# Kernel tuning notes

Hardware: AMD Instinct MI355X
Metric: run time of the kernel (lower is better)

The kernel has to match this reference:

```python
import jax, jax.numpy as jnp
import numpy as np


def setup_inputs() -> dict:
    key = jax.random.key(0)
    ks = jax.random.split(key, 6)
    B, L, D, E = 4, 2048, 1024, 4
    H = 4 * D
    x = jax.random.normal(ks[0], (B, L, D), dtype=jnp.float32)
    # router: Linear(D, 2D) -> GELU -> Linear(2D, E); kaiming-ish init
    rW1 = jax.random.normal(ks[1], (D, 2 * D), dtype=jnp.float32) * (2.0 / D) ** 0.5
    rb1 = jnp.zeros((2 * D,), dtype=jnp.float32)
    rW2 = jax.random.normal(ks[2], (2 * D, E), dtype=jnp.float32) * (2.0 / (2 * D)) ** 0.5
    rb2 = jnp.zeros((E,), dtype=jnp.float32)
    # experts: Linear(D, 4D) -> GELU -> Linear(4D, D), stacked over E
    We1 = jax.random.normal(ks[3], (E, D, H), dtype=jnp.float32) * (2.0 / D) ** 0.5
    be1 = jnp.zeros((E, H), dtype=jnp.float32)
    We2 = jax.random.normal(ks[4], (E, H, D), dtype=jnp.float32) * (2.0 / H) ** 0.5
    be2 = jnp.zeros((E, D), dtype=jnp.float32)
    return {"x": x, "rW1": rW1, "rb1": rb1, "rW2": rW2, "rb2": rb2,
            "We1": We1, "be1": be1, "We2": We2, "be2": be2}


def reference(x, rW1, rb1, rW2, rb2, We1, be1, We2, be2):
    E = We1.shape[0]
    top_k = min(2, E)
    # router (dropouts are identity in eval mode)
    rh = jax.nn.gelu(x @ rW1 + rb1, approximate=False)          # [B,L,2D]
    router_logits = rh @ rW2 + rb2                               # [B,L,E]
    router_probs = jax.nn.softmax(router_logits, axis=-1)
    expert_weights, expert_indices = jax.lax.top_k(router_probs, top_k)  # [B,L,k]
    one_hot = jax.nn.one_hot(expert_indices, E, dtype=x.dtype)   # [B,L,k,E]
    token_mask = one_hot.sum(axis=2)                             # [B,L,E] 1 if expert selected
    combine_w = (one_hot * expert_weights[..., None]).sum(axis=2)  # [B,L,E] gate weight per expert
    out = jnp.zeros_like(x)
    for e in range(E):  # fixed small expert count; dense per-expert MLP over all tokens (as original)
        xi = x * token_mask[..., e:e + 1]
        h = jax.nn.gelu(xi @ We1[e] + be1[e], approximate=False)  # [B,L,4D]
        yo = h @ We2[e] + be2[e]                                  # [B,L,D]
        out = out + yo * combine_w[..., e:e + 1]
    return out
```

## Files before the change

kernel.cpp:

```cpp
#include <hip/hip_runtime.h>
#include <math.h>


typedef short bf16x8 __attribute__((ext_vector_type(8)));
typedef float f32x4 __attribute__((ext_vector_type(4)));
typedef unsigned short u16;

__device__ __forceinline__ u16 f2bf(float f) {
  unsigned u = __float_as_uint(f);
  u += 0x7FFFu + ((u >> 16) & 1u);
  return (u16)(u >> 16);
}
__device__ __forceinline__ float bf2f(u16 s) {
  return __uint_as_float(((unsigned)s) << 16);
}
__device__ __forceinline__ float gelu_f(float x) {
  return 0.5f * x * (1.0f + erff(x * 0.70710678118654752f));
}
__device__ __forceinline__ float gelu_fast(float x) {
  float y = 1.5957691216057308f * (x + 0.044715f * x * x * x);
  float e = __expf(y);
  float t = 1.0f - 2.0f * __builtin_amdgcn_rcpf(e + 1.0f);
  return 0.5f * x * (1.0f + t);
}
__device__ __forceinline__ void gload_lds16(const void* g, void* l) {
  __builtin_amdgcn_global_load_lds(
      (const __attribute__((address_space(1))) void*)g,
      (__attribute__((address_space(3))) void*)l, 16, 0, 0);
}

__global__ __launch_bounds__(256) void convert_split_kernel(
    const float* __restrict__ in, u16* __restrict__ hi, u16* __restrict__ lo,
    int n4) {
  int i = blockIdx.x * blockDim.x + threadIdx.x;
  int stride = gridDim.x * blockDim.x;
  for (; i < n4; i += stride) {
    float4 v = ((const float4*)in)[i];
    float f[4] = {v.x, v.y, v.z, v.w};
    ushort4 h4, l4;
    u16* hp = (u16*)&h4;
    u16* lp = (u16*)&l4;
#pragma unroll
    for (int u = 0; u < 4; ++u) {
      u16 h = f2bf(f[u]);
      hp[u] = h;
      lp[u] = f2bf(f[u] - bf2f(h));
    }
    ((ushort4*)hi)[i] = h4;
    ((ushort4*)lo)[i] = l4;
  }
}

__global__ __launch_bounds__(256) void transpose_split_kernel(
    const float* __restrict__ in, u16* __restrict__ hi, u16* __restrict__ lo,
    int R, int C) {
  __shared__ float tile[32][33];
  const int c0 = blockIdx.x * 32, r0 = blockIdx.y * 32;
#pragma unroll
  for (int i = 0; i < 4; ++i) {
    int rr = threadIdx.y + i * 8;
    tile[rr][threadIdx.x] = in[(size_t)(r0 + rr) * C + c0 + threadIdx.x];
  }
  __syncthreads();
#pragma unroll
  for (int i = 0; i < 4; ++i) {
    int cc = threadIdx.y + i * 8;
    float v = tile[threadIdx.x][cc];
    u16 h = f2bf(v);
    size_t oidx = (size_t)(c0 + cc) * R + r0 + threadIdx.x;
    hi[oidx] = h;
    lo[oidx] = f2bf(v - bf2f(h));
  }
}

__global__ __launch_bounds__(256) void transpose_pair_kernel(
    const float* __restrict__ We1, const float* __restrict__ We2,
    u16* __restrict__ T1, u16* __restrict__ T2, size_t tstride, int e0) {
  __shared__ float tile[32][33];
  const int e = e0 + blockIdx.y;
  int b = blockIdx.x;
  const float* in;
  u16* out;
  int R, C, tx, ty;
  if (b < 4096) {
    in = We1 + (size_t)e * 1024 * 4096;
    out = T1 + (size_t)blockIdx.y * tstride;
    R = 1024; C = 4096; tx = b & 127; ty = b >> 7;
  } else {
    b -= 4096;
    in = We2 + (size_t)e * 1024 * 4096;
    out = T2 + (size_t)blockIdx.y * tstride;
    R = 4096; C = 1024; tx = b & 31; ty = b >> 5;
  }
  const int c0 = tx * 32, r0 = ty * 32;
#pragma unroll
  for (int i = 0; i < 4; ++i) {
    int rr = threadIdx.y + i * 8;
    tile[rr][threadIdx.x] = in[(size_t)(r0 + rr) * C + c0 + threadIdx.x];
  }
  __syncthreads();
#pragma unroll
  for (int i = 0; i < 4; ++i) {
    int cc = threadIdx.y + i * 8;
    out[(size_t)(c0 + cc) * R + r0 + threadIdx.x] = f2bf(tile[threadIdx.x][cc]);
  }
}

__global__ __launch_bounds__(256) void gemm3_router_kernel(
    const u16* __restrict__ Ahi, const u16* __restrict__ Alo,
    const u16* __restrict__ Bhi, const u16* __restrict__ Blo, int K,
    const float* __restrict__ bias, const float* __restrict__ rW2,
    float* __restrict__ parts) {
  __shared__ alignas(16) u16 Sm[4 * 128 * 32];
  __shared__ float pls[2][128][4];
  const int tid = threadIdx.x;
  const int lane = tid & 63;
  const int w = tid >> 6;
  const int wr = w >> 1, wc = w & 1;

  const int flat = blockIdx.x + blockIdx.y * 16;
  const int swz = (flat & 7) * 128 + (flat >> 3);
  const int bxs = swz & 15;
  const int bys = swz >> 4;
  const int brow = bys * 128;
  const int bcol = bxs * 128;

  f32x4 acc[4][4] = {};
  char* S = (char*)Sm;
  const u16* srcs[4] = {Ahi + (size_t)brow * K, Alo + (size_t)brow * K,
                        Bhi + (size_t)bcol * K, Blo + (size_t)bcol * K};
  const int rA = lane & 15;
  const int kg2 = (lane >> 4) * 16;

  const int nk = K >> 5;
  for (int kt = 0; kt < nk; ++kt) {
    const int k0 = kt << 5;
    __syncthreads();
#pragma unroll
    for (int i = 0; i < 8; ++i) {
      int c = tid + 256 * i;
      int tile = c >> 9;
      int cc = c & 511;
      int row = cc >> 2;
      int kp = (cc & 3) << 3;
      gload_lds16(srcs[tile] + (size_t)row * K + (k0 + kp), S + c * 16);
    }
    __syncthreads();

    bf16x8 ah[4], al[4], bh[4], bl[4];
#pragma unroll
    for (int m = 0; m < 4; ++m) {
      int ro = (wr * 64 + m * 16 + rA) * 64 + kg2;
      ah[m] = *(const bf16x8*)(S + ro);
      al[m] = *(const bf16x8*)(S + 8192 + ro);
    }
#pragma unroll
    for (int n = 0; n < 4; ++n) {
      int ro = (wc * 64 + n * 16 + rA) * 64 + kg2;
      bh[n] = *(const bf16x8*)(S + 16384 + ro);
      bl[n] = *(const bf16x8*)(S + 24576 + ro);
    }
#pragma unroll
    for (int m = 0; m < 4; ++m)
#pragma unroll
      for (int n = 0; n < 4; ++n) {
        acc[m][n] = __builtin_amdgcn_mfma_f32_16x16x32_bf16(ah[m], bh[n], acc[m][n], 0, 0, 0);
        acc[m][n] = __builtin_amdgcn_mfma_f32_16x16x32_bf16(al[m], bh[n], acc[m][n], 0, 0, 0);
        acc[m][n] = __builtin_amdgcn_mfma_f32_16x16x32_bf16(ah[m], bl[n], acc[m][n], 0, 0, 0);
      }
  }

  const int cr = (lane >> 4) * 4;
  const int ccx = lane & 15;
  float4 w2v[4];
  float bv[4];
#pragma unroll
  for (int n = 0; n < 4; ++n) {
    const int gc = bcol + wc * 64 + n * 16 + ccx;
    w2v[n] = ((const float4*)rW2)[gc];
    bv[n] = bias[gc];
  }
#pragma unroll
  for (int m = 0; m < 4; ++m) {
    float pl[4][4];
#pragma unroll
    for (int r = 0; r < 4; ++r)
#pragma unroll
      for (int e = 0; e < 4; ++e) pl[r][e] = 0.f;
#pragma unroll
    for (int n = 0; n < 4; ++n)
#pragma unroll
      for (int r = 0; r < 4; ++r) {
        const float v = gelu_f(acc[m][n][r] + bv[n]);
        pl[r][0] += v * w2v[n].x;
        pl[r][1] += v * w2v[n].y;
        pl[r][2] += v * w2v[n].z;
        pl[r][3] += v * w2v[n].w;
      }
#pragma unroll
    for (int off = 8; off; off >>= 1)
#pragma unroll
      for (int r = 0; r < 4; ++r)
#pragma unroll
        for (int e = 0; e < 4; ++e) pl[r][e] += __shfl_xor(pl[r][e], off);
    if ((lane & 15) == 0) {
      const int row = wr * 64 + m * 16 + cr;
#pragma unroll
      for (int r = 0; r < 4; ++r)
#pragma unroll
        for (int e = 0; e < 4; ++e) pls[wc][row + r][e] = pl[r][e];
    }
  }
  __syncthreads();
  for (int i = tid; i < 512; i += 256) {
    const int row = i >> 2, e = i & 3;
    parts[((size_t)bxs * 8192 + brow + row) * 4 + e] =
        pls[0][row][e] + pls[1][row][e];
  }
}

__global__ __launch_bounds__(256) void topk_kernel(
    const float* __restrict__ parts, const float* __restrict__ rb2,
    float* __restrict__ combine, int* __restrict__ cnt, int* __restrict__ list,
    int2* __restrict__ tokslot, int T) {
  const int t = blockIdx.x * 256 + threadIdx.x;
  const int w = threadIdx.x >> 6, lane = threadIdx.x & 63;
  __shared__ int wpre[4][4];
  __shared__ int gbase[4];

  float lg[4] = {rb2[0], rb2[1], rb2[2], rb2[3]};
#pragma unroll
  for (int s = 0; s < 16; ++s) {
    float4 pv = ((const float4*)parts)[(size_t)s * 8192 + t];
    lg[0] += pv.x;
    lg[1] += pv.y;
    lg[2] += pv.z;
    lg[3] += pv.w;
  }
  float mx = fmaxf(fmaxf(lg[0], lg[1]), fmaxf(lg[2], lg[3]));
  float p[4], sum = 0.f;
#pragma unroll
  for (int e = 0; e < 4; ++e) {
    p[e] = expf(lg[e] - mx);
    sum += p[e];
  }
  float inv = 1.0f / sum;
  int i1 = 0;
#pragma unroll
  for (int e = 1; e < 4; ++e)
    if (lg[e] > lg[i1]) i1 = e;
  int i2 = -1;
#pragma unroll
  for (int e = 0; e < 4; ++e)
    if (e != i1 && (i2 < 0 || lg[e] > lg[i2])) i2 = e;
  float4 cw = {0.f, 0.f, 0.f, 0.f};
  ((float*)&cw)[i1] = p[i1] * inv;
  ((float*)&cw)[i2] = p[i2] * inv;
  ((float4*)combine)[t] = cw;

  unsigned long long m[4];
#pragma unroll
  for (int e = 0; e < 4; ++e) m[e] = __ballot(i1 == e || i2 == e);
  if (lane == 0) {
#pragma unroll
    for (int e = 0; e < 4; ++e) wpre[w][e] = (int)__popcll(m[e]);
  }
  __syncthreads();
  if (threadIdx.x < 4) {
    const int e = threadIdx.x;
    int tot = 0;
#pragma unroll
    for (int ww = 0; ww < 4; ++ww) {
      int c = wpre[ww][e];
      wpre[ww][e] = tot;
      tot += c;
    }
    gbase[e] = atomicAdd(&cnt[e], tot);
  }
  __syncthreads();
  const unsigned long long lt = (1ull << lane) - 1ull;
  int p1 = gbase[i1] + wpre[w][i1] + (int)__popcll(m[i1] & lt);
  list[i1 * 8192 + p1] = t;
  int p2 = gbase[i2] + wpre[w][i2] + (int)__popcll(m[i2] & lt);
  list[i2 * 8192 + p2] = t;
  tokslot[t] = make_int2(i1 * 8192 + p1, i2 * 8192 + p2);
}

__global__ void prefix_kernel(const int* __restrict__ cnt, int* __restrict__ pre) {
  if (threadIdx.x == 0) {
    int s = 0;
#pragma unroll
    for (int e = 0; e < 4; ++e) {
      pre[e] = s;
      s += cnt[e];
    }
  }
}

__global__ __launch_bounds__(512) void gemm_gather_kernel(
    const u16* __restrict__ A, const u16* __restrict__ WT, size_t wts,
    const int* __restrict__ list, const int* __restrict__ cnt_arr,
    const int* __restrict__ hbase_arr, int e0, const float* __restrict__ be1,
    u16* __restrict__ h) {
  const int K = 1024;
  const int e = e0 + blockIdx.z;
  const int cnt = cnt_arr[e];
  const int rb = blockIdx.y;
  if (rb * 128 >= cnt) return;
  const int hbase = hbase_arr[e];
  const int* lst = list + e * 8192;
  const u16* Bt = WT + (size_t)blockIdx.z * wts;
  const float* bias = be1 + e * 4096;

  __shared__ alignas(16) u16 As[128 * 64];
  __shared__ alignas(16) u16 Bs[256 * 64];
  const int tid = threadIdx.x;
  const int lane = tid & 63;
  const int w = tid >> 6;
  const int wr = w >> 2, wc = w & 3;
  const int bcol = blockIdx.x * 256;

  const int srow = tid >> 3;
  const int jx8 = (((tid & 7) ^ (srow & 7)) << 3);
  const u16* aS[2];
  const u16* bS[4];
#pragma unroll
  for (int i = 0; i < 2; ++i) {
    int g = rb * 128 + srow + 64 * i;
    int tok = lst[(g < cnt) ? g : rb * 128];
    aS[i] = A + (size_t)tok * K + jx8;
  }
#pragma unroll
  for (int i = 0; i < 4; ++i)
    bS[i] = Bt + (size_t)(bcol + srow + 64 * i) * K + jx8;
  char* AsB = (char*)As;
  char* BsB = (char*)Bs;
  const int dstb = tid * 16;

  f32x4 acc[4][4] = {};
  const int rA = lane & 15;
  const int ksl = lane >> 4;
  const int rx7 = rA & 7;

  const int nk = K >> 6;
  for (int kt = 0; kt < nk; ++kt) {
    const int kb = kt << 6;
    __syncthreads();
#pragma unroll
    for (int i = 0; i < 2; ++i)
      gload_lds16(aS[i] + kb, AsB + i * 8192 + dstb);
#pragma unroll
    for (int i = 0; i < 4; ++i)
      gload_lds16(bS[i] + kb, BsB + i * 8192 + dstb);
    __syncthreads();
#pragma unroll
    for (int s = 0; s < 2; ++s) {
      bf16x8 a[4], b[4];
      const int sl = (((s * 4 + ksl) ^ rx7) << 4);
#pragma unroll
      for (int m = 0; m < 4; ++m)
        a[m] = *(const bf16x8*)(AsB + (wr * 64 + m * 16 + rA) * 128 + sl);
#pragma unroll
      for (int n = 0; n < 4; ++n)
        b[n] = *(const bf16x8*)(BsB + (wc * 64 + n * 16 + rA) * 128 + sl);
#pragma unroll
      for (int m = 0; m < 4; ++m)
#pragma unroll
        for (int n = 0; n < 4; ++n)
          acc[m][n] =
              __builtin_amdgcn_mfma_f32_16x16x32_bf16(a[m], b[n], acc[m][n], 0, 0, 0);
    }
  }

  const int cr = (lane >> 4) * 4;
  const int ccx = lane & 15;
#pragma unroll
  for (int m = 0; m < 4; ++m)
#pragma unroll
    for (int n = 0; n < 4; ++n) {
      const int gc = bcol + wc * 64 + n * 16 + ccx;
      const float bv = bias[gc];
#pragma unroll
      for (int r = 0; r < 4; ++r) {
        const int gl = rb * 128 + wr * 64 + m * 16 + cr + r;
        if (gl < cnt)
          h[(size_t)(hbase + gl) * 4096 + gc] = f2bf(gelu_fast(acc[m][n][r] + bv));
      }
    }
}

__global__ __launch_bounds__(512) void gemm_scatter_y_kernel(
    const u16* __restrict__ h, const int* __restrict__ hbase_arr,
    const u16* __restrict__ WT, size_t wts, const int* __restrict__ cnt_arr,
    int e0, const float* __restrict__ be2, u16* __restrict__ yout) {
  const int K = 4096;
  const int e = e0 + blockIdx.z;
  const int cnt = cnt_arr[e];
  const int rb = blockIdx.y;
  if (rb * 128 >= cnt) return;
  const int hbase = hbase_arr[e];
  const u16* Bt = WT + (size_t)blockIdx.z * wts;
  const float* bias = be2 + e * 1024;

  __shared__ alignas(16) u16 As[128 * 64];
  __shared__ alignas(16) u16 Bs[256 * 64];
  const int tid = threadIdx.x;
  const int lane = tid & 63;
  const int w = tid >> 6;
  const int wr = w >> 2, wc = w & 3;
  const int bcol = blockIdx.x * 256;

  const int srow = tid >> 3;
  const int jx8 = (((tid & 7) ^ (srow & 7)) << 3);
  const u16* aS[2];
  const u16* bS[4];
#pragma unroll
  for (int i = 0; i < 2; ++i)
    aS[i] = h + (size_t)(hbase + rb * 128 + srow + 64 * i) * K + jx8;
#pragma unroll
  for (int i = 0; i < 4; ++i)
    bS[i] = Bt + (size_t)(bcol + srow + 64 * i) * K + jx8;
  char* AsB = (char*)As;
  char* BsB = (char*)Bs;
  const int dstb = tid * 16;

  f32x4 acc[4][4] = {};
  const int rA = lane & 15;
  const int ksl = lane >> 4;
  const int rx7 = rA & 7;

  const int nk = K >> 6;
  for (int kt = 0; kt < nk; ++kt) {
    const int kb = kt << 6;
    __syncthreads();
#pragma unroll
    for (int i = 0; i < 2; ++i)
      gload_lds16(aS[i] + kb, AsB + i * 8192 + dstb);
#pragma unroll
    for (int i = 0; i < 4; ++i)
      gload_lds16(bS[i] + kb, BsB + i * 8192 + dstb);
    __syncthreads();
#pragma unroll
    for (int s = 0; s < 2; ++s) {
      bf16x8 a[4], b[4];
      const int sl = (((s * 4 + ksl) ^ rx7) << 4);
#pragma unroll
      for (int m = 0; m < 4; ++m)
        a[m] = *(const bf16x8*)(AsB + (wr * 64 + m * 16 + rA) * 128 + sl);
#pragma unroll
      for (int n = 0; n < 4; ++n)
        b[n] = *(const bf16x8*)(BsB + (wc * 64 + n * 16 + rA) * 128 + sl);
#pragma unroll
      for (int m = 0; m < 4; ++m)
#pragma unroll
        for (int n = 0; n < 4; ++n)
          acc[m][n] =
              __builtin_amdgcn_mfma_f32_16x16x32_bf16(a[m], b[n], acc[m][n], 0, 0, 0);
    }
  }

  const int cr = (lane >> 4) * 4;
  const int ccx = lane & 15;
#pragma unroll
  for (int m = 0; m < 4; ++m)
#pragma unroll
    for (int r = 0; r < 4; ++r) {
      const int gl = rb * 128 + wr * 64 + m * 16 + cr + r;
      if (gl >= cnt) continue;
      u16* yrow = yout + (size_t)(hbase + gl) * 1024;
#pragma unroll
      for (int n = 0; n < 4; ++n) {
        const int gc = bcol + wc * 64 + n * 16 + ccx;
        yrow[gc] = f2bf(acc[m][n][r] + bias[gc]);
      }
    }
}

__global__ __launch_bounds__(256) void combine_kernel(
    const u16* __restrict__ yout, const int2* __restrict__ tokslot,
    const int* __restrict__ prefix, const float* __restrict__ gates,
    float* __restrict__ out) {
  const int w = threadIdx.x >> 6, lane = threadIdx.x & 63;
  const int t = blockIdx.x * 4 + w;
  const int2 s = tokslot[t];
  const int e1 = s.x >> 13, p1 = s.x & 8191;
  const int e2 = s.y >> 13, p2 = s.y & 8191;
  const int r1 = prefix[e1] + p1;
  const int r2 = prefix[e2] + p2;
  const float g1 = gates[(size_t)t * 4 + e1];
  const float g2 = gates[(size_t)t * 4 + e2];
  const ushort4* y1 = (const ushort4*)(yout + (size_t)r1 * 1024);
  const ushort4* y2 = (const ushort4*)(yout + (size_t)r2 * 1024);
  float4* o = (float4*)(out + (size_t)t * 1024);
#pragma unroll
  for (int j = 0; j < 4; ++j) {
    const int c = lane + j * 64;
    ushort4 a = y1[c], b = y2[c];
    float4 r;
    r.x = g1 * bf2f(a.x) + g2 * bf2f(b.x);
    r.y = g1 * bf2f(a.y) + g2 * bf2f(b.y);
    r.z = g1 * bf2f(a.z) + g2 * bf2f(b.z);
    r.w = g1 * bf2f(a.w) + g2 * bf2f(b.w);
    o[c] = r;
  }
}

__global__ __launch_bounds__(512) void gemm_scatter_kernel(
    const u16* __restrict__ h, const int* __restrict__ hbase_arr,
    const u16* __restrict__ WT, size_t wts, const int* __restrict__ list,
    const int* __restrict__ cnt_arr, int e0, const float* __restrict__ be2,
    const float* __restrict__ combine, float* __restrict__ out) {
  const int K = 4096;
  const int zslot = blockIdx.z >> 1;
  const int kz = blockIdx.z & 1;
  const int e = e0 + zslot;
  const int cnt = cnt_arr[e];
  const int rb = blockIdx.y;
  if (rb * 128 >= cnt) return;
  const int hbase = hbase_arr[e];
  const int* lst = list + e * 8192;
  const u16* Bt = WT + (size_t)zslot * wts;
  const float* bias = be2 + e * 1024;
  const int koff = kz * 2048;

  __shared__ alignas(16) u16 As[128 * 64];
  __shared__ alignas(16) u16 Bs[256 * 64];
  const int tid = threadIdx.x;
  const int lane = tid & 63;
  const int w = tid >> 6;
  const int wr = w >> 2, wc = w & 3;
  const int bcol = blockIdx.x * 256;

  const int srow = tid >> 3;
  const int jx8 = (((tid & 7) ^ (srow & 7)) << 3);
  const u16* aS[2];
  const u16* bS[4];
#pragma unroll
  for (int i = 0; i < 2; ++i)
    aS[i] = h + (size_t)(hbase + rb * 128 + srow + 64 * i) * K + koff + jx8;
#pragma unroll
  for (int i = 0; i < 4; ++i)
    bS[i] = Bt + (size_t)(bcol + srow + 64 * i) * K + koff + jx8;
  char* AsB = (char*)As;
  char* BsB = (char*)Bs;
  const int dstb = tid * 16;

  f32x4 acc[4][4] = {};
  const int rA = lane & 15;
  const int ksl = lane >> 4;
  const int rx7 = rA & 7;

  const int nk = 2048 >> 6;
  for (int kt = 0; kt < nk; ++kt) {
    const int kb = kt << 6;
    __syncthreads();
#pragma unroll
    for (int i = 0; i < 2; ++i)
      gload_lds16(aS[i] + kb, AsB + i * 8192 + dstb);
#pragma unroll
    for (int i = 0; i < 4; ++i)
      gload_lds16(bS[i] + kb, BsB + i * 8192 + dstb);
    __syncthreads();
#pragma unroll
    for (int s = 0; s < 2; ++s) {
      bf16x8 a[4], b[4];
      const int sl = (((s * 4 + ksl) ^ rx7) << 4);
#pragma unroll
      for (int m = 0; m < 4; ++m)
        a[m] = *(const bf16x8*)(AsB + (wr * 64 + m * 16 + rA) * 128 + sl);
#pragma unroll
      for (int n = 0; n < 4; ++n)
        b[n] = *(const bf16x8*)(BsB + (wc * 64 + n * 16 + rA) * 128 + sl);
#pragma unroll
      for (int m = 0; m < 4; ++m)
#pragma unroll
        for (int n = 0; n < 4; ++n)
          acc[m][n] =
              __builtin_amdgcn_mfma_f32_16x16x32_bf16(a[m], b[n], acc[m][n], 0, 0, 0);
    }
  }

  const int cr = (lane >> 4) * 4;
  const int ccx = lane & 15;
  const bool addb = (kz == 0);
#pragma unroll
  for (int m = 0; m < 4; ++m)
#pragma unroll
    for (int r = 0; r < 4; ++r) {
      const int gl = rb * 128 + wr * 64 + m * 16 + cr + r;
      if (gl >= cnt) continue;
      const int tok = lst[gl];
      const float gcoef = combine[(size_t)tok * 4 + e];
      float* orow = out + (size_t)tok * 1024;
#pragma unroll
      for (int n = 0; n < 4; ++n) {
        const int gc = bcol + wc * 64 + n * 16 + ccx;
        float v = acc[m][n][r];
        if (addb) v += bias[gc];
        atomicAdd(&orow[gc], gcoef * v);
      }
    }
}

extern "C" void kernel_launch(void* const* d_in, const int* in_sizes, int n_in,
                              void* d_out, int out_size, void* d_ws,
                              size_t ws_size, hipStream_t stream) {
  const float* x = (const float*)d_in[0];
  const float* rW1 = (const float*)d_in[1];
  const float* rb1 = (const float*)d_in[2];
  const float* rW2 = (const float*)d_in[3];
  const float* rb2 = (const float*)d_in[4];
  const float* We1 = (const float*)d_in[5];
  const float* be1 = (const float*)d_in[6];
  const float* We2 = (const float*)d_in[7];
  const float* be2 = (const float*)d_in[8];
  float* out = (float*)d_out;

  const int T = 8192, D = 1024, D2 = 2048, H = 4096, E = 4;
  const size_t WTS = (size_t)H * D;

  char* ws = (char*)d_ws;
  size_t off = 0;
  auto alloc = [&](size_t bytes) {
    char* p = ws + off;
    off = (off + bytes + 255) & ~(size_t)255;
    return p;
  };
  u16* x_hi = (u16*)alloc((size_t)T * D * 2);
  float* combine = (float*)alloc((size_t)T * 4 * 4);
  int* cnt = (int*)alloc(256);
  int* prefix = cnt + 4;
  int* list = (int*)alloc((size_t)4 * 8192 * 4);
  int2* tokslot = (int2*)alloc((size_t)T * 8);
  const size_t common_off = off;

  bool merged;
  u16 *We1T, *We2T, *h, *x_lo, *rW1T_hi, *rW1T_lo, *yout;
  float* parts;
  {
    size_t o = common_off;
    auto a2 = [&](size_t bytes) {
      char* p = ws + o;
      o = (o + bytes + 255) & ~(size_t)255;
      return p;
    };
    u16* w1 = (u16*)a2((size_t)4 * WTS * 2);
    u16* w2 = (u16*)a2((size_t)4 * WTS * 2);
    char* hreg = a2((size_t)16384 * H * 2 + (2u << 20));
    merged = (o <= ws_size);
    if (merged) {
      We1T = w1;
      We2T = w2;
      h = (u16*)hreg;
      yout = w1;
      x_lo = (u16*)hreg;
      rW1T_hi = (u16*)(hreg + (16u << 20));
      rW1T_lo = (u16*)(hreg + (20u << 20));
      parts = (float*)(hreg + (24u << 20));
    }
  }
  if (!merged) {
    off = common_off;
    We1T = (u16*)alloc(WTS * 2);
    We2T = (u16*)alloc(WTS * 2);
    x_lo = (u16*)alloc((size_t)T * D * 2);
    rW1T_hi = (u16*)alloc((size_t)D2 * D * 2);
    rW1T_lo = (u16*)alloc((size_t)D2 * D * 2);
    parts = (float*)alloc((size_t)16 * T * 4 * 4);
    h = (u16*)alloc((size_t)T * H * 2);
    yout = nullptr;
  }

  hipMemsetAsync(cnt, 0, 32, stream);
  if (!merged) hipMemsetAsync(out, 0, (size_t)T * D * 4, stream);

  dim3 tb(32, 8);

  convert_split_kernel<<<2048, 256, 0, stream>>>(x, x_hi, x_lo, T * D / 4);
  transpose_split_kernel<<<dim3(D2 / 32, D / 32), tb, 0, stream>>>(
      rW1, rW1T_hi, rW1T_lo, D, D2);
  gemm3_router_kernel<<<dim3(16, 64), 256, 0, stream>>>(
      x_hi, x_lo, rW1T_hi, rW1T_lo, D, rb1, rW2, parts);
  topk_kernel<<<T / 256, 256, 0, stream>>>(parts, rb2, combine, cnt, list,
                                           tokslot, T);

  if (merged) {
    prefix_kernel<<<1, 64, 0, stream>>>(cnt, prefix);
    transpose_pair_kernel<<<dim3(8192, 4), tb, 0, stream>>>(
        We1, We2, We1T, We2T, WTS, 0);
    gemm_gather_kernel<<<dim3(16, 64, 4), 512, 0, stream>>>(
        x_hi, We1T, WTS, list, cnt, prefix, 0, be1, h);
    gemm_scatter_y_kernel<<<dim3(4, 64, 4), 512, 0, stream>>>(
        h, prefix, We2T, WTS, cnt, 0, be2, yout);
    combine_kernel<<<T / 4, 256, 0, stream>>>(yout, tokslot, prefix, combine,
                                              out);
  } else {
    for (int e = 0; e < E; ++e) {
      transpose_pair_kernel<<<dim3(8192, 1), tb, 0, stream>>>(
          We1, We2, We1T, We2T, 0, e);
      gemm_gather_kernel<<<dim3(16, 64, 1), 512, 0, stream>>>(
          x_hi, We1T, 0, list, cnt, prefix , e, be1, h);
      gemm_scatter_kernel<<<dim3(4, 64, 2), 512, 0, stream>>>(
          h, prefix , We2T, 0, list, cnt, e, be2, combine, out);
    }
  }
}
```

Measured before the change: 585.6 us.

## Double-buffer LDS tiles in expert GEMMs to overlap global loads with MFMA

Both expert GEMM kernels now keep two LDS stages and issue the async global-to-LDS loads for the next K tile before computing on the current one. Each stage waits on the vmcnt counter for only the older loads, then uses raw s_barrier calls instead of two __syncthreads per iteration. The goal is to hide global memory latency behind the MFMA work. In exchange, LDS use per block grows to 96KB, which lowers occupancy. It also relies on manual waitcnt accounting, so correctness hinges on the vmcnt value matching the six loads issued per stage.

Result: slower. 644.5 us (+10.1%).

```diff
diff --git a/kernel.cpp b/kernel.cpp
--- a/kernel.cpp
+++ b/kernel.cpp
@@ -312,8 +312,7 @@
   const u16* Bt = WT + (size_t)blockIdx.z * wts;
   const float* bias = be1 + e * 4096;
 
-  __shared__ alignas(16) u16 As[128 * 64];
-  __shared__ alignas(16) u16 Bs[256 * 64];
+  __shared__ alignas(16) char lds[98304];
   const int tid = threadIdx.x;
   const int lane = tid & 63;
   const int w = tid >> 6;
@@ -333,9 +332,17 @@
 #pragma unroll
   for (int i = 0; i < 4; ++i)
     bS[i] = Bt + (size_t)(bcol + srow + 64 * i) * K + jx8;
-  char* AsB = (char*)As;
-  char* BsB = (char*)Bs;
   const int dstb = tid * 16;
+
+#define G_STAGE(kt, buf)                                                   \
+  {                                                                        \
+    const int kb_ = (kt) << 6;                                             \
+    char* base_ = lds + (buf)*49152;                                       \
+    _Pragma("unroll") for (int i = 0; i < 2; ++i)                          \
+        gload_lds16(aS[i] + kb_, base_ + i * 8192 + dstb);                 \
+    _Pragma("unroll") for (int i = 0; i < 4; ++i)                          \
+        gload_lds16(bS[i] + kb_, base_ + 16384 + i * 8192 + dstb);         \
+  }
 
   f32x4 acc[4][4] = {};
   const int rA = lane & 15;
@@ -343,26 +350,28 @@
   const int rx7 = rA & 7;
 
   const int nk = K >> 6;
+  int cur = 0;
+  G_STAGE(0, 0);
   for (int kt = 0; kt < nk; ++kt) {
-    const int kb = kt << 6;
-    __syncthreads();
-#pragma unroll
-    for (int i = 0; i < 2; ++i)
-      gload_lds16(aS[i] + kb, AsB + i * 8192 + dstb);
-#pragma unroll
-    for (int i = 0; i < 4; ++i)
-      gload_lds16(bS[i] + kb, BsB + i * 8192 + dstb);
-    __syncthreads();
+    if (kt + 1 < nk) {
+      G_STAGE(kt + 1, cur ^ 1);
+      asm volatile("s_waitcnt vmcnt(6)" ::: "memory");
+    } else {
+      asm volatile("s_waitcnt vmcnt(0)" ::: "memory");
+    }
+    __builtin_amdgcn_s_barrier();
+    const char* Ab_ = lds + cur * 49152;
+    const char* Bb_ = Ab_ + 16384;
 #pragma unroll
     for (int s = 0; s < 2; ++s) {
       bf16x8 a[4], b[4];
       const int sl = (((s * 4 + ksl) ^ rx7) << 4);
 #pragma unroll
       for (int m = 0; m < 4; ++m)
-        a[m] = *(const bf16x8*)(AsB + (wr * 64 + m * 16 + rA) * 128 + sl);
+        a[m] = *(const bf16x8*)(Ab_ + (wr * 64 + m * 16 + rA) * 128 + sl);
 #pragma unroll
       for (int n = 0; n < 4; ++n)
-        b[n] = *(const bf16x8*)(BsB + (wc * 64 + n * 16 + rA) * 128 + sl);
+        b[n] = *(const bf16x8*)(Bb_ + (wc * 64 + n * 16 + rA) * 128 + sl);
 #pragma unroll
       for (int m = 0; m < 4; ++m)
 #pragma unroll
@@ -370,7 +379,10 @@
           acc[m][n] =
               __builtin_amdgcn_mfma_f32_16x16x32_bf16(a[m], b[n], acc[m][n], 0, 0, 0);
     }
-  }
+    __builtin_amdgcn_s_barrier();
+    cur ^= 1;
+  }
+#undef G_STAGE
 
   const int cr = (lane >> 4) * 4;
   const int ccx = lane & 15;
@@ -402,8 +414,7 @@
   const u16* Bt = WT + (size_t)blockIdx.z * wts;
   const float* bias = be2 + e * 1024;
 
-  __shared__ alignas(16) u16 As[128 * 64];
-  __shared__ alignas(16) u16 Bs[256 * 64];
+  __shared__ alignas(16) char lds[98304];
   const int tid = threadIdx.x;
   const int lane = tid & 63;
   const int w = tid >> 6;
@@ -420,9 +431,17 @@
 #pragma unroll
   for (int i = 0; i < 4; ++i)
     bS[i] = Bt + (size_t)(bcol + srow + 64 * i) * K + jx8;
-  char* AsB = (char*)As;
-  char* BsB = (char*)Bs;
   const int dstb = tid * 16;
+
+#define S_STAGE(kt, buf)                                                   \
+  {                                                                        \
+    const int kb_ = (kt) << 6;                                             \
+    char* base_ = lds + (buf)*49152;                                       \
+    _Pragma("unroll") for (int i = 0; i < 2; ++i)                          \
+        gload_lds16(aS[i] + kb_, base_ + i * 8192 + dstb);                 \
+    _Pragma("unroll") for (int i = 0; i < 4; ++i)                          \
+        gload_lds16(bS[i] + kb_, base_ + 16384 + i * 8192 + dstb);         \
+  }
 
   f32x4 acc[4][4] = {};
   const int rA = lane & 15;
@@ -430,26 +449,28 @@
   const int rx7 = rA & 7;
 
   const int nk = K >> 6;
+  int cur = 0;
+  S_STAGE(0, 0);
   for (int kt = 0; kt < nk; ++kt) {
-    const int kb = kt << 6;
-    __syncthreads();
-#pragma unroll
-    for (int i = 0; i < 2; ++i)
-      gload_lds16(aS[i] + kb, AsB + i * 8192 + dstb);
-#pragma unroll
-    for (int i = 0; i < 4; ++i)
-      gload_lds16(bS[i] + kb, BsB + i * 8192 + dstb);
-    __syncthreads();
+    if (kt + 1 < nk) {
+      S_STAGE(kt + 1, cur ^ 1);
+      asm volatile("s_waitcnt vmcnt(6)" ::: "memory");
+    } else {
+      asm volatile("s_waitcnt vmcnt(0)" ::: "memory");
+    }
+    __builtin_amdgcn_s_barrier();
+    const char* Ab_ = lds + cur * 49152;
+    const char* Bb_ = Ab_ + 16384;
 #pragma unroll
     for (int s = 0; s < 2; ++s) {
       bf16x8 a[4], b[4];
       const int sl = (((s * 4 + ksl) ^ rx7) << 4);
 #pragma unroll
       for (int m = 0; m < 4; ++m)
-        a[m] = *(const bf16x8*)(AsB + (wr * 64 + m * 16 + rA) * 128 + sl);
+        a[m] = *(const bf16x8*)(Ab_ + (wr * 64 + m * 16 + rA) * 128 + sl);
 #pragma unroll
       for (int n = 0; n < 4; ++n)
-        b[n] = *(const bf16x8*)(BsB + (wc * 64 + n * 16 + rA) * 128 + sl);
+        b[n] = *(const bf16x8*)(Bb_ + (wc * 64 + n * 16 + rA) * 128 + sl);
 #pragma unroll
       for (int m = 0; m < 4; ++m)
 #pragma unroll
@@ -457,7 +478,10 @@
           acc[m][n] =
               __builtin_amdgcn_mfma_f32_16x16x32_bf16(a[m], b[n], acc[m][n], 0, 0, 0);
     }
-  }
+    __builtin_amdgcn_s_barrier();
+    cur ^= 1;
+  }
+#undef S_STAGE
 
   const int cr = (lane >> 4) * 4;
   const int ccx = lane & 15;
```
